# Optimization experiments

Hardware: AMD Instinct MI355X
Metric: run time of the kernel (lower is better)

Reference implementation:

```python
import jax, jax.numpy as jnp
import numpy as np

BLOCK_SIZE = 8
SELECT_TOPK = 32
HIDDEN = 512
CHANNELS = 384
NUM_HEADS = 8
B, H, W = 8, 64, 64


def setup_inputs() -> dict:
    key = jax.random.key(0)
    ks = jax.random.split(key, 8)
    num_block_tot = (H // BLOCK_SIZE) * (W // BLOCK_SIZE)
    bs2 = BLOCK_SIZE * BLOCK_SIZE
    x = jax.random.normal(ks[0], (B, H, W, CHANNELS), dtype=jnp.float32)
    aw = jax.random.normal(ks[1], (NUM_HEADS, B, num_block_tot, bs2, bs2 + SELECT_TOPK), dtype=jnp.float32)
    attn_weights = jax.nn.softmax(aw, axis=-1)  # module expects sum(-1)==1
    weights = jax.random.uniform(ks[2], (B, num_block_tot, SELECT_TOPK), dtype=jnp.float32)
    indexes = jax.random.randint(ks[3], (B, num_block_tot, SELECT_TOPK), 0, H * W)
    in_proj_w = jax.random.normal(ks[4], (3 * HIDDEN, CHANNELS), dtype=jnp.float32) * 0.02
    in_proj_b = jax.random.normal(ks[5], (3 * HIDDEN,), dtype=jnp.float32) * 0.02
    out_proj_w = jax.random.normal(ks[6], (CHANNELS, HIDDEN), dtype=jnp.float32) * 0.02
    out_proj_b = jax.random.normal(ks[7], (CHANNELS,), dtype=jnp.float32) * 0.02
    return {"x": x, "attn_weights": attn_weights, "weights": weights,
            "in_proj_w": in_proj_w, "in_proj_b": in_proj_b,
            "out_proj_w": out_proj_w, "out_proj_b": out_proj_b,
            "indexes": indexes}


def reference(x, attn_weights, weights, in_proj_w, in_proj_b, out_proj_w, out_proj_b, indexes):
    batch, height, width, _ = x.shape
    bsz = BLOCK_SIZE
    nbh, nbw = height // bsz, width // bsz
    nbt = nbh * nbw
    num_heads = attn_weights.shape[0]
    hid = HIDDEN
    hd = hid // num_heads
    topk = SELECT_TOPK

    proj = jnp.einsum('bhwc,oc->bhwo', x, in_proj_w) + in_proj_b  # (B,H,W,3*hid)
    s, xh, y = jnp.split(proj, 3, axis=-1)
    xh = xh * jnp.tanh(s)  # Balancer/Whiten/Identity are identity in fwd

    # top-k gathered tokens: (B, nbt, topk, hid) without (B,nbt,num_tokens,hid) blowup
    x_flat = xh.reshape(batch, height * width, hid)
    sel = jax.vmap(lambda xf, ix: xf[ix])(x_flat, indexes)  # (B,nbt,topk,hid)
    sel = sel * weights[..., None]
    sel = sel.reshape(batch, nbt, topk, num_heads, hd).transpose(3, 0, 1, 2, 4)  # (nh,B,nbt,topk,hd)

    # block-local tokens: (nh, B, nbt, bsz^2, hd)
    blk = xh.reshape(batch, nbh, bsz, nbw, bsz, num_heads, hd)
    blk = blk.transpose(5, 0, 1, 3, 2, 4, 6).reshape(num_heads, batch, nbt, bsz * bsz, hd)

    kv = jnp.concatenate([blk, sel], axis=3)  # (nh,B,nbt,bsz^2+topk,hd)
    out = jnp.einsum('hbnqk,hbnkd->hbnqd', attn_weights, kv)  # (nh,B,nbt,bsz^2,hd)

    out = out.reshape(num_heads, batch, nbh, nbw, bsz, bsz, hd)
    out = out.transpose(1, 2, 4, 3, 5, 0, 6).reshape(batch, height, width, hid)
    out = out * y
    return jnp.einsum('bhwd,cd->bhwc', out, out_proj_w) + out_proj_b
```

## Files before the change

### kernel.cpp

```cpp
#include <hip/hip_runtime.h>
#include <hip/hip_bf16.h>
#include <stdint.h>

#define CH   384
#define HID  512
#define NHD  8
#define MTOT 32768

typedef __attribute__((ext_vector_type(8))) short bf16x8;
typedef __attribute__((ext_vector_type(4))) float f32x4;
typedef unsigned short u16;

__device__ __forceinline__ float bf2f(u16 v){ return __uint_as_float(((unsigned)v)<<16); }
__device__ __forceinline__ u16 f2bf(float f){
  unsigned u = __float_as_uint(f);
  return (u16)((u + 0x7fffu + ((u>>16)&1u)) >> 16);
}
__device__ __forceinline__ void gload_lds16(const void* g, void* l){
  __builtin_amdgcn_global_load_lds((const __attribute__((address_space(1))) void*)g,
                                   (__attribute__((address_space(3))) void*)l, 16, 0, 0);
}

__global__ void k_cvt(const float* __restrict__ in, u16* __restrict__ out, int n4){
  int i = blockIdx.x*blockDim.x + threadIdx.x;
  int stride = gridDim.x*blockDim.x;
  for (; i < n4; i += stride){
    float4 v = ((const float4*)in)[i];
    ushort4 o; o.x=f2bf(v.x); o.y=f2bf(v.y); o.z=f2bf(v.z); o.w=f2bf(v.w);
    ((ushort4*)out)[i] = o;
  }
}

__global__ void k_gemm1(const u16* __restrict__ xb, const u16* __restrict__ w1b,
                        const float* __restrict__ b1,
                        u16* __restrict__ xh, u16* __restrict__ yb)
{
  __shared__ short lA[128*64];
  __shared__ short lB[96*64];
  const int tid = threadIdx.x;
  const int w = tid >> 6, lw = tid & 63;
  const int m0 = blockIdx.x * 128;
  const int h0 = blockIdx.y * 32;

  f32x4 acc[2][6] = {};

  for (int kt = 0; kt < CH/64; ++kt){
    const int kbase = kt*64;
    #pragma unroll
    for (int i = 0; i < 4; ++i){
      int chunk = i*4 + w;
      int row = chunk*8 + (lw>>3);
      int sl  = (lw&7) ^ (row&7);
      gload_lds16(xb + (size_t)(m0+row)*CH + kbase + sl*8, &lA[chunk*512]);
    }
    #pragma unroll
    for (int i = 0; i < 3; ++i){
      int chunk = i*4 + w;
      int row = chunk*8 + (lw>>3);
      int grow = (row>>5)*HID + h0 + (row&31);
      int sl = (lw&7) ^ (row&7);
      gload_lds16(w1b + (size_t)grow*CH + kbase + sl*8, &lB[chunk*512]);
    }
    __syncthreads();
    #pragma unroll
    for (int ks = 0; ks < 2; ++ks){
      bf16x8 af[2], bfr[6];
      #pragma unroll
      for (int mi=0; mi<2; ++mi){
        int row = w*32 + mi*16 + (lw&15);
        int sl = (ks*4 + (lw>>4)) ^ (row&7);
        af[mi] = *(const bf16x8*)&lA[row*64 + sl*8];
      }
      #pragma unroll
      for (int nj=0; nj<6; ++nj){
        int row = nj*16 + (lw&15);
        int sl = (ks*4 + (lw>>4)) ^ (row&7);
        bfr[nj] = *(const bf16x8*)&lB[row*64 + sl*8];
      }
      #pragma unroll
      for (int mi=0; mi<2; ++mi)
        #pragma unroll
        for (int nj=0; nj<6; ++nj)
          acc[mi][nj] = __builtin_amdgcn_mfma_f32_16x16x32_bf16(af[mi], bfr[nj], acc[mi][nj], 0,0,0);
    }
    __syncthreads();
  }

  const int lc = lw & 15, lr4 = (lw>>4)*4;
  #pragma unroll
  for (int f=0; f<2; ++f){
    int col = h0 + f*16 + lc;
    float bs = b1[col], bx = b1[512+col], by = b1[1024+col];
    #pragma unroll
    for (int mi=0; mi<2; ++mi){
      #pragma unroll
      for (int j=0; j<4; ++j){
        int row = m0 + w*32 + mi*16 + lr4 + j;
        float s  = acc[mi][0+f][j] + bs;
        float xv = (acc[mi][2+f][j] + bx) * tanhf(s);
        float yv = acc[mi][4+f][j] + by;
        xh[(size_t)row*HID + col] = f2bf(xv);
        yb[(size_t)row*HID + col] = f2bf(yv);
      }
    }
  }
}

__global__ __launch_bounds__(64, 3)
void k_attn(const float* __restrict__ aw, const float* __restrict__ wts,
            const int* __restrict__ idxs,
            const u16* __restrict__ xh, const u16* __restrict__ yb,
            u16* __restrict__ zb)
{
  __shared__ short lKv[64*96];
  const int tid = threadIdx.x;
  const int bid = blockIdx.x;
  const int h = bid >> 9;
  const int b = (bid >> 6) & 7;
  const int n = bid & 63;
  const int bh = n >> 3, bw = n & 7;

  {
    const int dg = tid & 7;
    const int pr = tid >> 3;
    #pragma unroll
    for (int it = 0; it < 6; ++it){
      int pair = it*8 + pr;
      int t0 = pair*2;
      size_t r0, r1;
      if (t0 < 64){
        int pix = (bh*8 + (t0>>3))*64 + bw*8 + (t0&7);
        r0 = (size_t)b*4096 + pix;
        r1 = r0 + 1;
      } else {
        int e = (b*64+n)*32 + (t0-64);
        r0 = (size_t)b*4096 + idxs[e];
        r1 = (size_t)b*4096 + idxs[e+1];
      }
      bf16x8 v0 = *(const bf16x8*)&xh[r0*HID + h*64 + dg*8];
      bf16x8 v1 = *(const bf16x8*)&xh[r1*HID + h*64 + dg*8];
      #pragma unroll
      for (int j = 0; j < 8; ++j){
        int d = dg*8 + j;
        int elem = (d*96 + t0) ^ (dg<<3);
        unsigned pk = (unsigned)(u16)v0[j] | ((unsigned)(u16)v1[j] << 16);
        *(unsigned*)&lKv[elem] = pk;
      }
    }
  }

  float wv[8];
  {
    const float* wp = wts + (size_t)(b*64+n)*32 + (tid>>4)*8;
    float4 a = *(const float4*)wp, c = *(const float4*)(wp+4);
    wv[0]=a.x; wv[1]=a.y; wv[2]=a.z; wv[3]=a.w;
    wv[4]=c.x; wv[5]=c.y; wv[6]=c.z; wv[7]=c.w;
  }
  const float* awp = aw + (size_t)bid * (64*96);
  bf16x8 af[3][4];
  #pragma unroll
  for (int ks = 0; ks < 3; ++ks){
    #pragma unroll
    for (int mi = 0; mi < 4; ++mi){
      const float* p = awp + (size_t)(mi*16 + (tid&15))*96 + ks*32 + (tid>>4)*8;
      float4 f0 = *(const float4*)p;
      float4 f1 = *(const float4*)(p+4);
      float t[8] = {f0.x,f0.y,f0.z,f0.w,f1.x,f1.y,f1.z,f1.w};
      #pragma unroll
      for (int j = 0; j < 8; ++j){
        float v = (ks == 2) ? t[j]*wv[j] : t[j];
        af[ks][mi][j] = (short)f2bf(v);
      }
    }
  }
  __syncthreads();

  f32x4 acc[4][4] = {};
  const int lc = tid & 15, lk = tid >> 4;
  #pragma unroll
  for (int ks = 0; ks < 3; ++ks){
    bf16x8 bv[4];
    #pragma unroll
    for (int nj = 0; nj < 4; ++nj){
      int d = nj*16 + lc;
      int idx = (d*96 + ks*32 + lk*8) ^ ((d>>3)<<3);
      bv[nj] = *(const bf16x8*)&lKv[idx];
    }
    #pragma unroll
    for (int mi = 0; mi < 4; ++mi)
      #pragma unroll
      for (int nj = 0; nj < 4; ++nj)
        acc[mi][nj] = __builtin_amdgcn_mfma_f32_16x16x32_bf16(af[ks][mi], bv[nj], acc[mi][nj], 0,0,0);
  }

  #pragma unroll
  for (int mi = 0; mi < 4; ++mi){
    #pragma unroll
    for (int nj = 0; nj < 4; ++nj){
      int d = nj*16 + lc;
      size_t gcol = (size_t)h*64 + d;
      #pragma unroll
      for (int j = 0; j < 4; ++j){
        int q = mi*16 + lk*4 + j;
        int pix = (bh*8 + (q>>3))*64 + bw*8 + (q&7);
        size_t r = (size_t)b*4096 + pix;
        float yv = bf2f(yb[r*HID + gcol]);
        zb[r*HID + gcol] = f2bf(acc[mi][nj][j] * yv);
      }
    }
  }
}

__global__ void k_gemm2(const u16* __restrict__ zb, const u16* __restrict__ w2b,
                        const float* __restrict__ b2, float* __restrict__ out)
{
  __shared__ short lA[128*64];
  __shared__ short lB[128*64];
  const int tid = threadIdx.x;
  const int w = tid>>6, lw = tid&63;
  const int wm = w>>1, wn = w&1;
  const int m0 = blockIdx.x*128, n0 = blockIdx.y*128;

  f32x4 acc[4][4] = {};

  for (int kt=0; kt<HID/64; ++kt){
    int kbase = kt*64;
    #pragma unroll
    for (int i=0; i<4; ++i){
      int chunk = i*4 + w;
      int row = chunk*8 + (lw>>3);
      int sl = (lw&7) ^ (row&7);
      gload_lds16(zb  + (size_t)(m0+row)*HID + kbase + sl*8, &lA[chunk*512]);
      gload_lds16(w2b + (size_t)(n0+row)*HID + kbase + sl*8, &lB[chunk*512]);
    }
    __syncthreads();
    #pragma unroll
    for (int ks=0; ks<2; ++ks){
      bf16x8 af[4], bb[4];
      #pragma unroll
      for (int mi=0; mi<4; ++mi){
        int row = wm*64 + mi*16 + (lw&15);
        int sl = (ks*4 + (lw>>4)) ^ (row&7);
        af[mi] = *(const bf16x8*)&lA[row*64 + sl*8];
      }
      #pragma unroll
      for (int nj=0; nj<4; ++nj){
        int row = wn*64 + nj*16 + (lw&15);
        int sl = (ks*4 + (lw>>4)) ^ (row&7);
        bb[nj] = *(const bf16x8*)&lB[row*64 + sl*8];
      }
      #pragma unroll
      for (int mi=0; mi<4; ++mi)
        #pragma unroll
        for (int nj=0; nj<4; ++nj)
          acc[mi][nj] = __builtin_amdgcn_mfma_f32_16x16x32_bf16(af[mi], bb[nj], acc[mi][nj], 0,0,0);
    }
    __syncthreads();
  }

  const int lc = lw&15, lr4 = (lw>>4)*4;
  #pragma unroll
  for (int nj=0; nj<4; ++nj){
    int col = n0 + wn*64 + nj*16 + lc;
    float bias = b2[col];
    #pragma unroll
    for (int mi=0; mi<4; ++mi){
      #pragma unroll
      for (int j=0; j<4; ++j){
        int row = m0 + wm*64 + mi*16 + lr4 + j;
        out[(size_t)row*CH + col] = acc[mi][nj][j] + bias;
      }
    }
  }
}

extern "C" void kernel_launch(void* const* d_in, const int* in_sizes, int n_in,
                              void* d_out, int out_size, void* d_ws, size_t ws_size,
                              hipStream_t stream) {
  const float* x   = (const float*)d_in[0];
  const float* aw  = (const float*)d_in[1];
  const float* wts = (const float*)d_in[2];
  const float* w1  = (const float*)d_in[3];
  const float* b1  = (const float*)d_in[4];
  const float* w2  = (const float*)d_in[5];
  const float* b2  = (const float*)d_in[6];
  const int*   idx = (const int*)d_in[7];
  float* out = (float*)d_out;

  char* ws = (char*)d_ws;
  u16* x_bf  = (u16*)(ws);
  u16* w1_bf = (u16*)(ws + 25165824);
  u16* w2_bf = (u16*)(ws + 26345472);
  u16* xh_bf = (u16*)(ws + 26738688);
  u16* y_bf  = (u16*)(ws + 60293120);
  u16* z_bf  = (u16*)(ws + 93847552);

  k_cvt<<<2048, 256, 0, stream>>>(x,  x_bf,  MTOT*CH/4);
  k_cvt<<<576,  256, 0, stream>>>(w1, w1_bf, 3*HID*CH/4);
  k_cvt<<<192,  256, 0, stream>>>(w2, w2_bf, CH*HID/4);

  k_gemm1<<<dim3(MTOT/128, HID/32), 256, 0, stream>>>(x_bf, w1_bf, b1, xh_bf, y_bf);
  k_attn<<<NHD*8*64, 64, 0, stream>>>(aw, wts, idx, xh_bf, y_bf, z_bf);
  k_gemm2<<<dim3(MTOT/128, CH/128), 256, 0, stream>>>(z_bf, w2_bf, b2, out);
}
```

Before: 151.1 us.

## Double-buffer gemm1 K loop, enlarge N tile, and stage epilogue through LDS

Restructures the first projection GEMM. It uses a larger 128x(3x64) tile with a 2x2 wave layout and a K step of 32, double-buffered so that async global-to-LDS loads for the next step overlap the MFMA work on the current one. The epilogue now writes the gated x and y values to LDS and then emits coalesced 16-byte row stores instead of scattered 2-byte stores. The aim is to hide load latency, halve the number of A-tile reloads, and improve write coalescing, at the cost of more accumulator registers and lower occupancy.

```diff
diff --git a/kernel.cpp b/kernel.cpp
--- a/kernel.cpp
+++ b/kernel.cpp
@@ -31,77 +31,107 @@
   }
 }
 
-__global__ void k_gemm1(const u16* __restrict__ xb, const u16* __restrict__ w1b,
-                        const float* __restrict__ b1,
-                        u16* __restrict__ xh, u16* __restrict__ yb)
+__global__ __launch_bounds__(256)
+void k_gemm1(const u16* __restrict__ xb, const u16* __restrict__ w1b,
+             const float* __restrict__ b1,
+             u16* __restrict__ xh, u16* __restrict__ yb)
 {
-  __shared__ short lA[128*64];
-  __shared__ short lB[96*64];
+  __shared__ short lds[20480];
   const int tid = threadIdx.x;
   const int w = tid >> 6, lw = tid & 63;
+  const int wm = w >> 1, wn = w & 1;
   const int m0 = blockIdx.x * 128;
-  const int h0 = blockIdx.y * 32;
-
-  f32x4 acc[2][6] = {};
-
-  for (int kt = 0; kt < CH/64; ++kt){
-    const int kbase = kt*64;
-    #pragma unroll
-    for (int i = 0; i < 4; ++i){
-      int chunk = i*4 + w;
-      int row = chunk*8 + (lw>>3);
-      int sl  = (lw&7) ^ (row&7);
-      gload_lds16(xb + (size_t)(m0+row)*CH + kbase + sl*8, &lA[chunk*512]);
-    }
-    #pragma unroll
-    for (int i = 0; i < 3; ++i){
-      int chunk = i*4 + w;
-      int row = chunk*8 + (lw>>3);
-      int grow = (row>>5)*HID + h0 + (row&31);
-      int sl = (lw&7) ^ (row&7);
-      gload_lds16(w1b + (size_t)grow*CH + kbase + sl*8, &lB[chunk*512]);
-    }
+  const int h0 = blockIdx.y * 64;
+  const int lc = lw & 15, lk = lw >> 4;
+
+  f32x4 acc[4][6] = {};
+
+  const u16* gsrc[5]; int ldst[5]; int lstr[5];
+  {
+    const int sl = ((lw & 3) ^ ((lw >> 2) & 3)) * 8;
+    #pragma unroll
+    for (int i = 0; i < 5; ++i){
+      int c = w*5 + i;
+      if (c < 8){
+        int r = c*16 + (lw >> 2);
+        gsrc[i] = xb + (size_t)(m0 + r)*CH + sl;
+        ldst[i] = c*512; lstr[i] = 4096;
+      } else {
+        int cb = c - 8;
+        int grow = (cb % 3)*HID + h0 + (cb/3)*16 + (lw >> 2);
+        gsrc[i] = w1b + (size_t)grow*CH + sl;
+        ldst[i] = 8192 + cb*512; lstr[i] = 6144;
+      }
+    }
+  }
+  auto STAGE = [&](int buf, int kt){
+    #pragma unroll
+    for (int i = 0; i < 5; ++i)
+      gload_lds16(gsrc[i] + kt*32, &lds[ldst[i] + buf*lstr[i]]);
+  };
+
+  const int sA = (lk ^ (lc & 3)) * 8;
+  auto COMPUTE = [&](const short* pa, const short* pb){
+    bf16x8 af[4], bv[6];
+    #pragma unroll
+    for (int mi = 0; mi < 4; ++mi)
+      af[mi] = *(const bf16x8*)&pa[(wm*64 + mi*16 + lc)*32 + sA];
+    #pragma unroll
+    for (int nj = 0; nj < 6; ++nj)
+      bv[nj] = *(const bf16x8*)&pb[(wn*96 + (nj/3)*48 + (nj%3)*16 + lc)*32 + sA];
+    #pragma unroll
+    for (int mi = 0; mi < 4; ++mi)
+      #pragma unroll
+      for (int nj = 0; nj < 6; ++nj)
+        acc[mi][nj] = __builtin_amdgcn_mfma_f32_16x16x32_bf16(af[mi], bv[nj], acc[mi][nj], 0,0,0);
+  };
+
+  STAGE(0, 0);
+  __syncthreads();
+  #pragma unroll 1
+  for (int kt2 = 0; kt2 < 6; ++kt2){
+    STAGE(1, 2*kt2 + 1);
+    COMPUTE(lds + 0, lds + 8192);
     __syncthreads();
-    #pragma unroll
-    for (int ks = 0; ks < 2; ++ks){
-      bf16x8 af[2], bfr[6];
-      #pragma unroll
-      for (int mi=0; mi<2; ++mi){
-        int row = w*32 + mi*16 + (lw&15);
-        int sl = (ks*4 + (lw>>4)) ^ (row&7);
-        af[mi] = *(const bf16x8*)&lA[row*64 + sl*8];
-      }
-      #pragma unroll
-      for (int nj=0; nj<6; ++nj){
-        int row = nj*16 + (lw&15);
-        int sl = (ks*4 + (lw>>4)) ^ (row&7);
-        bfr[nj] = *(const bf16x8*)&lB[row*64 + sl*8];
-      }
-      #pragma unroll
-      for (int mi=0; mi<2; ++mi)
+    if (kt2 < 5) STAGE(0, 2*kt2 + 2);
+    COMPUTE(lds + 4096, lds + 14336);
+    __syncthreads();
+  }
+
+  __syncthreads();
+  {
+    short* ep  = &lds[w*2560];
+    short* ep2 = &lds[10240 + w*2560];
+    const int gr = m0 + wm*64 + lw;
+    const int gc = h0 + wn*32;
+    float bs[2], bx[2], by[2];
+    #pragma unroll
+    for (int hb = 0; hb < 2; ++hb){
+      int col = gc + hb*16 + lc;
+      bs[hb] = b1[col]; bx[hb] = b1[512 + col]; by[hb] = b1[1024 + col];
+    }
+    #pragma unroll
+    for (int mi = 0; mi < 4; ++mi)
+      #pragma unroll
+      for (int hb = 0; hb < 2; ++hb)
         #pragma unroll
-        for (int nj=0; nj<6; ++nj)
-          acc[mi][nj] = __builtin_amdgcn_mfma_f32_16x16x32_bf16(af[mi], bfr[nj], acc[mi][nj], 0,0,0);
-    }
-    __syncthreads();
-  }
-
-  const int lc = lw & 15, lr4 = (lw>>4)*4;
-  #pragma unroll
-  for (int f=0; f<2; ++f){
-    int col = h0 + f*16 + lc;
-    float bs = b1[col], bx = b1[512+col], by = b1[1024+col];
-    #pragma unroll
-    for (int mi=0; mi<2; ++mi){
-      #pragma unroll
-      for (int j=0; j<4; ++j){
-        int row = m0 + w*32 + mi*16 + lr4 + j;
-        float s  = acc[mi][0+f][j] + bs;
-        float xv = (acc[mi][2+f][j] + bx) * tanhf(s);
-        float yv = acc[mi][4+f][j] + by;
-        xh[(size_t)row*HID + col] = f2bf(xv);
-        yb[(size_t)row*HID + col] = f2bf(yv);
-      }
+        for (int j = 0; j < 4; ++j){
+          float sv = acc[mi][hb*3 + 0][j] + bs[hb];
+          float xv = (acc[mi][hb*3 + 1][j] + bx[hb]) * tanhf(sv);
+          float yv = acc[mi][hb*3 + 2][j] + by[hb];
+          int row = mi*16 + lk*4 + j;
+          ep [row*40 + hb*16 + lc] = (short)f2bf(xv);
+          ep2[row*40 + hb*16 + lc] = (short)f2bf(yv);
+        }
+    #pragma unroll
+    for (int q = 0; q < 4; ++q){
+      bf16x8 v = *(const bf16x8*)&ep[lw*40 + q*8];
+      *(bf16x8*)&xh[(size_t)gr*HID + gc + q*8] = v;
+    }
+    #pragma unroll
+    for (int q = 0; q < 4; ++q){
+      bf16x8 v = *(const bf16x8*)&ep2[lw*40 + q*8];
+      *(bf16x8*)&yb[(size_t)gr*HID + gc + q*8] = v;
     }
   }
 }
@@ -299,7 +329,7 @@
   k_cvt<<<576,  256, 0, stream>>>(w1, w1_bf, 3*HID*CH/4);
   k_cvt<<<192,  256, 0, stream>>>(w2, w2_bf, CH*HID/4);
 
-  k_gemm1<<<dim3(MTOT/128, HID/32), 256, 0, stream>>>(x_bf, w1_bf, b1, xh_bf, y_bf);
+  k_gemm1<<<dim3(MTOT/128, HID/64), 256, 0, stream>>>(x_bf, w1_bf, b1, xh_bf, y_bf);
   k_attn<<<NHD*8*64, 64, 0, stream>>>(aw, wts, idx, xh_bf, y_bf, z_bf);
   k_gemm2<<<dim3(MTOT/128, CH/128), 256, 0, stream>>>(z_bf, w2_bf, b2, out);
 }
```

After: 174.2 us. 1.15x slower.
